# Optimization experiments

Hardware: AMD Instinct MI355X
Metric: run time of the kernel (lower is better)

The kernel has to match this reference:

```python
import jax, jax.numpy as jnp
import numpy as np

N, G, E, H, OUT, MAX_N = 131072, 256, 384, 6, 256, 1024
DH = E // H  # 64


def _make_sizes():
    # variable-length segments summing exactly to N, each in [1, MAX_N]
    rng = np.random.default_rng(0)
    raw = rng.integers(128, 896, G).astype(np.int64)
    diff = int(N - raw.sum())
    q, r = divmod(diff, G)
    sizes = raw + q
    sizes[:r] += 1
    assert sizes.sum() == N and sizes.min() >= 1 and sizes.max() <= MAX_N
    return sizes


def setup_inputs() -> dict:
    key = jax.random.key(0)
    ks = jax.random.split(key, 8)
    s = 1.0 / np.sqrt(E)
    return {
        "node_feat": jax.random.normal(ks[0], (N, E), jnp.float32),
        "sizes": jnp.asarray(_make_sizes(), jnp.int32),
        "query": jax.random.normal(ks[1], (E,), jnp.float32),
        "Wq": jax.random.normal(ks[2], (E, E), jnp.float32) * s,
        "bq": jnp.zeros((E,), jnp.float32),
        "Wk": jax.random.normal(ks[3], (E, E), jnp.float32) * s,
        "bk": jnp.zeros((E,), jnp.float32),
        "Wv": jax.random.normal(ks[4], (E, E), jnp.float32) * s,
        "bv": jnp.zeros((E,), jnp.float32),
        "Wo": jax.random.normal(ks[5], (E, E), jnp.float32) * s,
        "bo": jnp.zeros((E,), jnp.float32),
        "Wp": jax.random.normal(ks[6], (OUT, E), jnp.float32) * s,
        "bp": jnp.zeros((OUT,), jnp.float32),
    }


def reference(node_feat, sizes, query, Wq, bq, Wk, bk, Wv, bv, Wo, bo, Wp, bp):
    # segment offsets and padded gather indices
    offsets = jnp.cumsum(sizes) - sizes                      # [G]
    pos = jnp.arange(MAX_N)
    idx = jnp.clip(offsets[:, None] + pos[None, :], 0, N - 1)  # [G, MAX_N]
    mask = pos[None, :] < sizes[:, None]                     # [G, MAX_N]

    # project K/V on the flat node table (one big GEMM), then gather into padded form
    k_flat = node_feat @ Wk.T + bk                           # [N, E]
    v_flat = node_feat @ Wv.T + bv
    k = k_flat[idx].reshape(G, MAX_N, H, DH)
    v = v_flat[idx].reshape(G, MAX_N, H, DH)

    # single shared query token, pre-scaled (PyTorch MHA scales q by 1/sqrt(head_dim))
    q = ((query @ Wq.T + bq) * (1.0 / np.sqrt(DH))).reshape(H, DH)

    scores = jnp.einsum('hd,gnhd->ghn', q, k)                # [G, H, MAX_N]
    scores = jnp.where(mask[:, None, :], scores, -1e30)
    attn = jax.nn.softmax(scores, axis=-1)
    pooled = jnp.einsum('ghn,gnhd->ghd', attn, v).reshape(G, E)

    out = pooled @ Wo.T + bo                                 # MHA out_proj
    return out @ Wp.T + bp                                   # final proj  [G, OUT]
```

## Files before the change

kernel.cpp:

```cpp
#include <hip/hip_runtime.h>
#include <math.h>

#define NN 131072
#define G  256
#define E  384
#define H  6
#define DH 64
#define OUTD 256
#define MAXN 1024

#define CHK 256
#define SLOTS 4
#define PART_STRIDE 2316

#define WS_QK   0
#define WS_C    2304
#define WS_OFF  2432
#define WS_QV   2944
#define WS_PART 4096
#define WS_WVT  (WS_PART + G*SLOTS*PART_STRIDE)
#define WS_WOT  (WS_WVT + E*E)
#define WS_WPT  (WS_WOT + E*E)

__global__ __launch_bounds__(256) void k0a_scan_qv(
    const int* __restrict__ sizes, const float* __restrict__ query,
    const float* __restrict__ Wq, const float* __restrict__ bq,
    float* __restrict__ wsf) {
  __shared__ int s_scan[G];
  const int tid = threadIdx.x;
  if (blockIdx.x == 0) {
    s_scan[tid] = sizes[tid];
    __syncthreads();
    for (int d = 1; d < G; d <<= 1) {
      int t = (tid >= d) ? s_scan[tid - d] : 0;
      __syncthreads();
      s_scan[tid] += t;
      __syncthreads();
    }
    int* offs = (int*)(wsf + WS_OFF);
    offs[tid] = s_scan[tid] - sizes[tid];
  } else {
    const int lane = tid & 63;
    const int i = (blockIdx.x - 1) * 4 + (tid >> 6);
    float a = 0.f;
#pragma unroll
    for (int j = 0; j < 6; j++)
      a += Wq[(size_t)i * E + j * 64 + lane] * query[j * 64 + lane];
#pragma unroll
    for (int mm = 1; mm < 64; mm <<= 1) a += __shfl_xor(a, mm, 64);
    if (lane == 0) wsf[WS_QV + i] = 0.125f * (a + bq[i]);
  }
}

__global__ __launch_bounds__(256) void k0b_qk(
    const float* __restrict__ Wk, const float* __restrict__ bk,
    float* __restrict__ wsf) {
  __shared__ float qv_s[64];
  __shared__ float ps[256];
  const int h = blockIdx.x / 6, ec = blockIdx.x % 6;
  const int tid = threadIdx.x;
  if (tid < 64) qv_s[tid] = wsf[WS_QV + h * 64 + tid];
  __syncthreads();
  const int el = tid & 63, dq = tid >> 6;
  float a = 0.f;
#pragma unroll 4
  for (int d = dq * 16; d < dq * 16 + 16; d++)
    a += qv_s[d] * Wk[(size_t)(h * 64 + d) * E + ec * 64 + el];
  ps[tid] = a;
  __syncthreads();
  if (tid < 64)
    wsf[WS_QK + h * E + ec * 64 + tid] =
        ps[tid] + ps[64 + tid] + ps[128 + tid] + ps[192 + tid];
  if (ec == 0 && tid < 64) {
    float p = qv_s[tid] * bk[h * 64 + tid];
#pragma unroll
    for (int mm = 1; mm < 64; mm <<= 1) p += __shfl_xor(p, mm, 64);
    if (tid == 0) wsf[WS_C + h] = p;
  }
}

__global__ __launch_bounds__(256) void k0t_transpose(
    const float* __restrict__ Wv, const float* __restrict__ Wo,
    const float* __restrict__ Wp, float* __restrict__ wsf) {
  __shared__ float s[64][65];
  const int b = blockIdx.x;
  const float* src;
  float* dst;
  int R, tr, tc;
  if (b < 36)      { src = Wv; dst = wsf + WS_WVT; R = 384; tr = b / 6;        tc = b % 6; }
  else if (b < 72) { src = Wo; dst = wsf + WS_WOT; R = 384; tr = (b - 36) / 6; tc = (b - 36) % 6; }
  else             { src = Wp; dst = wsf + WS_WPT; R = 256; tr = (b - 72) / 6; tc = (b - 72) % 6; }
  const int r0 = tr * 64, c0 = tc * 64;
#pragma unroll
  for (int k = 0; k < 16; k++) {
    int idx = k * 256 + threadIdx.x;
    int r = idx >> 6, cc = idx & 63;
    s[r][cc] = src[(size_t)(r0 + r) * E + c0 + cc];
  }
  __syncthreads();
#pragma unroll
  for (int k = 0; k < 16; k++) {
    int idx = k * 256 + threadIdx.x;
    int cc = idx >> 6, r = idx & 63;
    dst[(size_t)(c0 + cc) * R + r0 + r] = s[r][cc];
  }
}

#define PB 264
__global__ __launch_bounds__(512) void k12_fused(
    const float* __restrict__ x, const int* __restrict__ sizes,
    float* __restrict__ wsf) {
  __shared__ float qk_l[8 * 292];
  __shared__ float c_s[8];
  __shared__ float pbuf[H * PB];
  __shared__ float psum[4][H][128];
  const int g = blockIdx.x & 255, s = blockIdx.x >> 8;
  const int Ng = sizes[g];
  const int rem = Ng - s * CHK;
  if (rem <= 0) return;
  const int clen = rem < CHK ? rem : CHK;
  const int n0 = ((const int*)(wsf + WS_OFF))[g] + s * CHK;
  const int tid = threadIdx.x;

  for (int idx = tid; idx < 2304; idx += 512) {
    int sub = idx / 288, r3 = idx % 288;
    int h = r3 / 48, r2 = r3 % 48, j = r2 >> 2, r = r2 & 3;
    qk_l[sub * 292 + h * 48 + j * 4 + r] =
        wsf[WS_QK + h * E + (j * 8 + sub) * 4 + r];
  }
  if (tid < 8) c_s[tid] = (tid < 6) ? wsf[WS_C + tid] : 0.f;
  __syncthreads();

  const int lane = tid & 63, w = tid >> 6;
  const int sub = lane & 7, nod = lane >> 3;
  const float4* x4 = (const float4*)x;
  {
    const int base = w * 32;
    float acc[4][6];
#pragma unroll
    for (int o = 0; o < 4; o++)
#pragma unroll
      for (int h = 0; h < 6; h++) acc[o][h] = 0.f;
#pragma unroll 4
    for (int j = 0; j < 12; j++) {
      float4 qk4[6];
#pragma unroll
      for (int h = 0; h < 6; h++)
        qk4[h] = *(const float4*)&qk_l[sub * 292 + h * 48 + j * 4];
      float4 xv[4];
#pragma unroll
      for (int o = 0; o < 4; o++) {
        int nn = base + o * 8 + nod;
        nn = nn < clen ? nn : clen - 1;
        xv[o] = x4[(size_t)(n0 + nn) * 96 + j * 8 + sub];
      }
#pragma unroll
      for (int o = 0; o < 4; o++)
#pragma unroll
        for (int h = 0; h < 6; h++)
          acc[o][h] += qk4[h].x * xv[o].x + qk4[h].y * xv[o].y
                     + qk4[h].z * xv[o].z + qk4[h].w * xv[o].w;
    }
#pragma unroll
    for (int o = 0; o < 4; o++) {
#pragma unroll
      for (int h = 0; h < 6; h++) {
        acc[o][h] += __shfl_xor(acc[o][h], 1, 64);
        acc[o][h] += __shfl_xor(acc[o][h], 2, 64);
        acc[o][h] += __shfl_xor(acc[o][h], 4, 64);
      }
      float v = acc[o][0];
#pragma unroll
      for (int h = 1; h < 6; h++) v = (sub == h) ? acc[o][h] : v;
      if (sub < 6) {
        int nn = base + o * 8 + nod;
        pbuf[sub * PB + nn] = (nn < clen) ? v + c_s[sub] : -1.0e30f;
      }
    }
  }
  __syncthreads();

  float* pslot = wsf + WS_PART + (size_t)(g * SLOTS + s) * PART_STRIDE;
  if (w < 6) {
    float vals[4];
#pragma unroll
    for (int k = 0; k < 4; k++) vals[k] = pbuf[w * PB + lane + k * 64];
    float m = fmaxf(fmaxf(vals[0], vals[1]), fmaxf(vals[2], vals[3]));
#pragma unroll
    for (int mm = 1; mm < 64; mm <<= 1) m = fmaxf(m, __shfl_xor(m, mm, 64));
    float lsum = 0.f;
#pragma unroll
    for (int k = 0; k < 4; k++) {
      float e = __expf(vals[k] - m);
      pbuf[w * PB + lane + k * 64] = e;
      lsum += e;
    }
#pragma unroll
    for (int mm = 1; mm < 64; mm <<= 1) lsum += __shfl_xor(lsum, mm, 64);
    if (lane == 0) { pslot[2304 + w] = m; pslot[2310 + w] = lsum; }
  }
  __syncthreads();

  const int col = tid & 127, np = tid >> 7;
  for (int c = 0; c < 3; c++) {
    float acc[6];
#pragma unroll
    for (int h = 0; h < 6; h++) acc[h] = 0.f;
    const float* xcol = x + (size_t)n0 * E + c * 128 + col;
    for (int n = np * 64; n < np * 64 + 64; n += 8) {
      float xv[8];
#pragma unroll
      for (int k = 0; k < 8; k++) {
        int nn = n + k;
        nn = nn < clen ? nn : clen - 1;
        xv[k] = xcol[(size_t)nn * E];
      }
#pragma unroll
      for (int h = 0; h < 6; h++) {
        const float4 p0 = *(const float4*)&pbuf[h * PB + n];
        const float4 p1 = *(const float4*)&pbuf[h * PB + n + 4];
        acc[h] += p0.x * xv[0] + p0.y * xv[1] + p0.z * xv[2] + p0.w * xv[3]
                + p1.x * xv[4] + p1.y * xv[5] + p1.z * xv[6] + p1.w * xv[7];
      }
    }
#pragma unroll
    for (int h = 0; h < 6; h++) psum[np][h][col] = acc[h];
    __syncthreads();
    if (np == 0)
#pragma unroll
      for (int h = 0; h < 6; h++)
        pslot[h * E + c * 128 + col] =
            psum[0][h][col] + psum[1][h][col] + psum[2][h][col] + psum[3][h][col];
    __syncthreads();
  }
}

__global__ __launch_bounds__(768) void k3_group(
    const float* __restrict__ wsf, const int* __restrict__ sizes,
    const float* __restrict__ bv, const float* __restrict__ bo,
    const float* __restrict__ bp, float* __restrict__ out) {
  __shared__ float xb[H * E];
  __shared__ float pooled[E];
  __shared__ float om[E];
  __shared__ float ps[768];
  __shared__ float wgt[SLOTS][H];
  __shared__ float linv[H];
  const int tid = threadIdx.x;
  const int g = blockIdx.x;
  const int nch = (sizes[g] + CHK - 1) / CHK;
  const float* pg = wsf + WS_PART + (size_t)g * SLOTS * PART_STRIDE;
  const float* wvt = wsf + WS_WVT;
  const float* wot = wsf + WS_WOT;
  const float* wpt = wsf + WS_WPT;

  if (tid < H) {
    float m = -3.0e38f;
    for (int s = 0; s < nch; s++)
      m = fmaxf(m, pg[(size_t)s * PART_STRIDE + 2304 + tid]);
    float L = 0.f;
    for (int s = 0; s < nch; s++) {
      float wv_ = __expf(pg[(size_t)s * PART_STRIDE + 2304 + tid] - m);
      wgt[s][tid] = wv_;
      L += pg[(size_t)s * PART_STRIDE + 2310 + tid] * wv_;
    }
    linv[tid] = 1.f / L;
  }
  __syncthreads();
  for (int idx = tid; idx < H * E; idx += 768) {
    int h = idx / E;
    float a = 0.f;
    for (int s = 0; s < nch; s++) a += pg[(size_t)s * PART_STRIDE + idx] * wgt[s][h];
    xb[idx] = a * linv[h];
  }
  __syncthreads();

  {
    const int i = tid % 384, ks = tid / 384;
    const float* xh = xb + (i >> 6) * E + ks * 192;
    const float* wp_ = wvt + (size_t)(ks * 192) * E + i;
    float a0 = 0.f, a1 = 0.f, a2 = 0.f, a3 = 0.f;
#pragma unroll 4
    for (int e = 0; e < 192; e += 4) {
      a0 += wp_[(size_t)(e + 0) * E] * xh[e + 0];
      a1 += wp_[(size_t)(e + 1) * E] * xh[e + 1];
      a2 += wp_[(size_t)(e + 2) * E] * xh[e + 2];
      a3 += wp_[(size_t)(e + 3) * E] * xh[e + 3];
    }
    ps[tid] = (a0 + a1) + (a2 + a3);
  }
  __syncthreads();
  if (tid < 384) pooled[tid] = ps[tid] + ps[384 + tid] + bv[tid];
  __syncthreads();

  {
    const int i = tid % 384, ks = tid / 384;
    const float* xh = pooled + ks * 192;
    const float* wp_ = wot + (size_t)(ks * 192) * E + i;
    float a0 = 0.f, a1 = 0.f, a2 = 0.f, a3 = 0.f;
#pragma unroll 4
    for (int e = 0; e < 192; e += 4) {
      a0 += wp_[(size_t)(e + 0) * E] * xh[e + 0];
      a1 += wp_[(size_t)(e + 1) * E] * xh[e + 1];
      a2 += wp_[(size_t)(e + 2) * E] * xh[e + 2];
      a3 += wp_[(size_t)(e + 3) * E] * xh[e + 3];
    }
    ps[tid] = (a0 + a1) + (a2 + a3);
  }
  __syncthreads();
  if (tid < 384) om[tid] = ps[tid] + ps[384 + tid] + bo[tid];
  __syncthreads();

  {
    const int o = tid % 256, ks = tid / 256;
    const float* xh = om + ks * 128;
    const float* wp_ = wpt + (size_t)(ks * 128) * OUTD + o;
    float a0 = 0.f, a1 = 0.f, a2 = 0.f, a3 = 0.f;
#pragma unroll 4
    for (int e = 0; e < 128; e += 4) {
      a0 += wp_[(size_t)(e + 0) * OUTD] * xh[e + 0];
      a1 += wp_[(size_t)(e + 1) * OUTD] * xh[e + 1];
      a2 += wp_[(size_t)(e + 2) * OUTD] * xh[e + 2];
      a3 += wp_[(size_t)(e + 3) * OUTD] * xh[e + 3];
    }
    ps[tid] = (a0 + a1) + (a2 + a3);
  }
  __syncthreads();
  if (tid < 256)
    out[(size_t)g * OUTD + tid] = ps[tid] + ps[256 + tid] + ps[512 + tid] + bp[tid];
}

extern "C" void kernel_launch(void* const* d_in, const int* in_sizes, int n_in,
                              void* d_out, int out_size, void* d_ws, size_t ws_size,
                              hipStream_t stream) {
  const float* x     = (const float*)d_in[0];
  const int*   sizes = (const int*)d_in[1];
  const float* query = (const float*)d_in[2];
  const float* Wq    = (const float*)d_in[3];
  const float* bq    = (const float*)d_in[4];
  const float* Wk    = (const float*)d_in[5];
  const float* bk    = (const float*)d_in[6];
  const float* Wv    = (const float*)d_in[7];
  const float* bv    = (const float*)d_in[8];
  const float* Wo    = (const float*)d_in[9];
  const float* bo    = (const float*)d_in[10];
  const float* Wp    = (const float*)d_in[11];
  const float* bp    = (const float*)d_in[12];
  float* wsf = (float*)d_ws;
  float* out = (float*)d_out;

  hipLaunchKernelGGL(k0a_scan_qv, dim3(97), dim3(256), 0, stream,
                     sizes, query, Wq, bq, wsf);
  hipLaunchKernelGGL(k0b_qk, dim3(36), dim3(256), 0, stream, Wk, bk, wsf);
  hipLaunchKernelGGL(k0t_transpose, dim3(96), dim3(256), 0, stream,
                     Wv, Wo, Wp, wsf);
  hipLaunchKernelGGL(k12_fused, dim3(G * SLOTS), dim3(512), 0, stream,
                     x, sizes, wsf);
  hipLaunchKernelGGL(k3_group, dim3(G), dim3(768), 0, stream,
                     wsf, sizes, bv, bo, bp, out);
}
```

Before: 373.2 us.

## Use compact chunk worklist with 128-node chunks and float4 pooling

Segments are split into 128-node chunks instead of 256. A prefix scan builds a compact worklist of (group, chunk) items, so blocks map only to real chunks instead of early-exiting on empty slots. The weighted-sum stage now reads x as float4 rows with 192 threads and does a two-way partial reduction through reused shared memory. The finalize kernel finds each group's partial base with a serial per-block prefix sum. The trade-off is more partials to combine and extra serial work in k3.

```diff
diff --git a/kernel.cpp b/kernel.cpp
--- a/kernel.cpp
+++ b/kernel.cpp
@@ -9,15 +9,17 @@
 #define OUTD 256
 #define MAXN 1024
 
-#define CHK 256
-#define SLOTS 4
+#define CHK 128
+#define SLOTS 8
 #define PART_STRIDE 2316
 
 #define WS_QK   0
 #define WS_C    2304
 #define WS_OFF  2432
 #define WS_QV   2944
-#define WS_PART 4096
+#define WS_WL   3328
+#define WS_M    5376
+#define WS_PART 5632
 #define WS_WVT  (WS_PART + G*SLOTS*PART_STRIDE)
 #define WS_WOT  (WS_WVT + E*E)
 #define WS_WPT  (WS_WOT + E*E)
@@ -26,19 +28,29 @@
     const int* __restrict__ sizes, const float* __restrict__ query,
     const float* __restrict__ Wq, const float* __restrict__ bq,
     float* __restrict__ wsf) {
-  __shared__ int s_scan[G];
   const int tid = threadIdx.x;
   if (blockIdx.x == 0) {
-    s_scan[tid] = sizes[tid];
+    __shared__ int s_scan[G];
+    __shared__ int s_scan2[G];
+    const int sz = sizes[tid];
+    s_scan[tid] = sz;
+    const int nch = (sz + CHK - 1) >> 7;
+    s_scan2[tid] = nch;
     __syncthreads();
     for (int d = 1; d < G; d <<= 1) {
       int t = (tid >= d) ? s_scan[tid - d] : 0;
+      int t2 = (tid >= d) ? s_scan2[tid - d] : 0;
       __syncthreads();
       s_scan[tid] += t;
+      s_scan2[tid] += t2;
       __syncthreads();
     }
     int* offs = (int*)(wsf + WS_OFF);
-    offs[tid] = s_scan[tid] - sizes[tid];
+    offs[tid] = s_scan[tid] - sz;
+    int* wl = (int*)(wsf + WS_WL);
+    const int pos = s_scan2[tid] - nch;
+    for (int s = 0; s < nch; s++) wl[pos + s] = (tid << 3) | s;
+    if (tid == G - 1) ((int*)(wsf + WS_M))[0] = s_scan2[G - 1];
   } else {
     const int lane = tid & 63;
     const int i = (blockIdx.x - 1) * 4 + (tid >> 6);
@@ -106,23 +118,25 @@
   }
 }
 
-#define PB 264
-__global__ __launch_bounds__(512) void k12_fused(
+#define PB 136
+__global__ __launch_bounds__(256) void k12_fused(
     const float* __restrict__ x, const int* __restrict__ sizes,
     float* __restrict__ wsf) {
-  __shared__ float qk_l[8 * 292];
+  __shared__ float u_mem[4608];
+  __shared__ float pbuf[H * PB];
   __shared__ float c_s[8];
-  __shared__ float pbuf[H * PB];
-  __shared__ float psum[4][H][128];
-  const int g = blockIdx.x & 255, s = blockIdx.x >> 8;
+  const int M = ((const int*)(wsf + WS_M))[0];
+  if ((int)blockIdx.x >= M) return;
+  const int item = ((const int*)(wsf + WS_WL))[blockIdx.x];
+  const int g = item >> 3, s = item & 7;
   const int Ng = sizes[g];
   const int rem = Ng - s * CHK;
-  if (rem <= 0) return;
   const int clen = rem < CHK ? rem : CHK;
   const int n0 = ((const int*)(wsf + WS_OFF))[g] + s * CHK;
   const int tid = threadIdx.x;
 
-  for (int idx = tid; idx < 2304; idx += 512) {
+  float* qk_l = u_mem;
+  for (int idx = tid; idx < 2304; idx += 256) {
     int sub = idx / 288, r3 = idx % 288;
     int h = r3 / 48, r2 = r3 % 48, j = r2 >> 2, r = r2 & 3;
     qk_l[sub * 292 + h * 48 + j * 4 + r] =
@@ -180,59 +194,60 @@
   }
   __syncthreads();
 
-  float* pslot = wsf + WS_PART + (size_t)(g * SLOTS + s) * PART_STRIDE;
-  if (w < 6) {
-    float vals[4];
-#pragma unroll
-    for (int k = 0; k < 4; k++) vals[k] = pbuf[w * PB + lane + k * 64];
-    float m = fmaxf(fmaxf(vals[0], vals[1]), fmaxf(vals[2], vals[3]));
+  float* pslot = wsf + WS_PART + (size_t)blockIdx.x * PART_STRIDE;
+  for (int h = w; h < 6; h += 4) {
+    float v0 = pbuf[h * PB + lane], v1 = pbuf[h * PB + 64 + lane];
+    float m = fmaxf(v0, v1);
 #pragma unroll
     for (int mm = 1; mm < 64; mm <<= 1) m = fmaxf(m, __shfl_xor(m, mm, 64));
-    float lsum = 0.f;
-#pragma unroll
-    for (int k = 0; k < 4; k++) {
-      float e = __expf(vals[k] - m);
-      pbuf[w * PB + lane + k * 64] = e;
-      lsum += e;
-    }
-#pragma unroll
-    for (int mm = 1; mm < 64; mm <<= 1) lsum += __shfl_xor(lsum, mm, 64);
-    if (lane == 0) { pslot[2304 + w] = m; pslot[2310 + w] = lsum; }
-  }
-  __syncthreads();
-
-  const int col = tid & 127, np = tid >> 7;
-  for (int c = 0; c < 3; c++) {
-    float acc[6];
-#pragma unroll
-    for (int h = 0; h < 6; h++) acc[h] = 0.f;
-    const float* xcol = x + (size_t)n0 * E + c * 128 + col;
-    for (int n = np * 64; n < np * 64 + 64; n += 8) {
-      float xv[8];
-#pragma unroll
-      for (int k = 0; k < 8; k++) {
-        int nn = n + k;
+    float e0 = __expf(v0 - m), e1 = __expf(v1 - m);
+    pbuf[h * PB + lane] = e0;
+    pbuf[h * PB + 64 + lane] = e1;
+    float l = e0 + e1;
+#pragma unroll
+    for (int mm = 1; mm < 64; mm <<= 1) l += __shfl_xor(l, mm, 64);
+    if (lane == 0) { pslot[2304 + h] = m; pslot[2310 + h] = l; }
+  }
+  __syncthreads();
+
+  float* psum = u_mem;
+  if (tid < 192) {
+    const int f4 = tid % 96, np = tid / 96;
+    float acc[6][4];
+#pragma unroll
+    for (int h = 0; h < 6; h++)
+#pragma unroll
+      for (int c = 0; c < 4; c++) acc[h][c] = 0.f;
+#pragma unroll 2
+    for (int n = 0; n < 64; n += 4) {
+      float4 xv[4];
+#pragma unroll
+      for (int k = 0; k < 4; k++) {
+        int nn = np * 64 + n + k;
         nn = nn < clen ? nn : clen - 1;
-        xv[k] = xcol[(size_t)nn * E];
+        xv[k] = x4[(size_t)(n0 + nn) * 96 + f4];
       }
 #pragma unroll
       for (int h = 0; h < 6; h++) {
-        const float4 p0 = *(const float4*)&pbuf[h * PB + n];
-        const float4 p1 = *(const float4*)&pbuf[h * PB + n + 4];
-        acc[h] += p0.x * xv[0] + p0.y * xv[1] + p0.z * xv[2] + p0.w * xv[3]
-                + p1.x * xv[4] + p1.y * xv[5] + p1.z * xv[6] + p1.w * xv[7];
-      }
-    }
-#pragma unroll
-    for (int h = 0; h < 6; h++) psum[np][h][col] = acc[h];
-    __syncthreads();
-    if (np == 0)
-#pragma unroll
-      for (int h = 0; h < 6; h++)
-        pslot[h * E + c * 128 + col] =
-            psum[0][h][col] + psum[1][h][col] + psum[2][h][col] + psum[3][h][col];
-    __syncthreads();
-  }
+        const float4 p = *(const float4*)&pbuf[h * PB + np * 64 + n];
+#pragma unroll
+        for (int c = 0; c < 4; c++) {
+          const float* xc = (const float*)&xv[0];
+        }
+        acc[h][0] += p.x * xv[0].x + p.y * xv[1].x + p.z * xv[2].x + p.w * xv[3].x;
+        acc[h][1] += p.x * xv[0].y + p.y * xv[1].y + p.z * xv[2].y + p.w * xv[3].y;
+        acc[h][2] += p.x * xv[0].z + p.y * xv[1].z + p.z * xv[2].z + p.w * xv[3].z;
+        acc[h][3] += p.x * xv[0].w + p.y * xv[1].w + p.z * xv[2].w + p.w * xv[3].w;
+      }
+    }
+#pragma unroll
+    for (int h = 0; h < 6; h++)
+      *(float4*)&psum[(np * 6 + h) * E + f4 * 4] =
+          make_float4(acc[h][0], acc[h][1], acc[h][2], acc[h][3]);
+  }
+  __syncthreads();
+  for (int idx = tid; idx < 2304; idx += 256)
+    pslot[idx] = psum[idx] + psum[2304 + idx];
 }
 
 __global__ __launch_bounds__(768) void k3_group(
@@ -245,10 +260,17 @@
   __shared__ float ps[768];
   __shared__ float wgt[SLOTS][H];
   __shared__ float linv[H];
+  __shared__ int base_s;
   const int tid = threadIdx.x;
   const int g = blockIdx.x;
-  const int nch = (sizes[g] + CHK - 1) / CHK;
-  const float* pg = wsf + WS_PART + (size_t)g * SLOTS * PART_STRIDE;
+  const int nch = (sizes[g] + CHK - 1) >> 7;
+  if (tid == 0) {
+    int b = 0;
+    for (int gg = 0; gg < g; gg++) b += (sizes[gg] + CHK - 1) >> 7;
+    base_s = b;
+  }
+  __syncthreads();
+  const float* pg = wsf + WS_PART + (size_t)base_s * PART_STRIDE;
   const float* wvt = wsf + WS_WVT;
   const float* wot = wsf + WS_WOT;
   const float* wpt = wsf + WS_WPT;
@@ -353,7 +375,7 @@
   hipLaunchKernelGGL(k0b_qk, dim3(36), dim3(256), 0, stream, Wk, bk, wsf);
   hipLaunchKernelGGL(k0t_transpose, dim3(96), dim3(256), 0, stream,
                      Wv, Wo, Wp, wsf);
-  hipLaunchKernelGGL(k12_fused, dim3(G * SLOTS), dim3(512), 0, stream,
+  hipLaunchKernelGGL(k12_fused, dim3(G * SLOTS), dim3(256), 0, stream,
                      x, sizes, wsf);
   hipLaunchKernelGGL(k3_group, dim3(G), dim3(768), 0, stream,
                      wsf, sizes, bv, bo, bp, out);
```

Result: no change. 373.3 us (+0.0%).
